# Performance work log

Hardware: AMD Instinct MI355X
Metric: run time of the kernel (lower is better)

Reference implementation:

```python
import jax, jax.numpy as jnp
import numpy as np

MAX_ITERS = 20
TOL = 1e-6
STEP = 1.0
EPS = 1e-7
CLIP = 1e-7


def _normalize(x, axis=-1):
    n = jnp.linalg.norm(x, axis=axis, keepdims=True)
    return x / jnp.maximum(n, 1e-12)


def _safe_acos(x):
    return jnp.arccos(jnp.clip(x, -1.0 + CLIP, 1.0 - CLIP))


def setup_inputs() -> dict:
    key = jax.random.key(0)
    NC, K, N, D = 1000, 8, 32, 128
    X_groups = jax.random.normal(key, (NC, K, N, D), dtype=jnp.float32)
    return {"X_groups": X_groups}


def reference(X_groups):
    # X_groups: (NC, K, N, D)
    NC, K, N, D = X_groups.shape
    X = X_groups.reshape(NC * K, N, D)
    Xn = _normalize(X)                      # (G, N, D) unit vectors
    mu = _normalize(jnp.mean(Xn, axis=1))   # (G, D) init mean

    done = jnp.array(False)
    for _ in range(MAX_ITERS):
        dots = jnp.einsum('gd,gnd->gn', mu, Xn)             # (G, N)
        theta = _safe_acos(dots)
        sin_t = jnp.maximum(jnp.sin(theta), EPS)
        diff = Xn - dots[..., None] * mu[:, None, :]        # (G, N, D)
        log_vecs = (theta / sin_t)[..., None] * diff        # log map
        v = jnp.mean(log_vecs, axis=1)                      # (G, D)
        v_norm = jnp.maximum(jnp.linalg.norm(v, axis=-1, keepdims=True), EPS)
        done = done | (jnp.max(v_norm) < TOL)               # global convergence (as in torch .item() check)
        v_step = STEP * v
        vs_norm = jnp.maximum(jnp.linalg.norm(v_step, axis=-1, keepdims=True), EPS)
        mu_new = jnp.cos(vs_norm) * mu + jnp.sin(vs_norm) * (v_step / vs_norm)  # exp map
        mu_new = _normalize(mu_new)
        mu = jnp.where(done, mu, mu_new)

    # calc_cluster_distance: features (G, N, D) @ means (G, D)
    sims = jnp.einsum('gnd,gd->gn', Xn, mu)
    sims = jnp.clip(sims, -1 + CLIP, 1 - CLIP)
    loss = jnp.mean(jnp.sum(jnp.arccos(sims) ** 2, axis=-1))
    return loss
```

## Files before the change

kernel.cpp:

```cpp
#include <hip/hip_runtime.h>
#include <stdint.h>

#define MAX_ITERS 20
#define EPSV 1e-7f
#define CLIPV 1e-7f
#define PI_F 3.14159265358979f
#define PIO2_F 1.57079632679490f

typedef __attribute__((ext_vector_type(8))) short short8;
typedef __attribute__((ext_vector_type(4))) float f4;

__device__ __forceinline__ f4 mfma_bf16(short8 a, short8 b, f4 c) {
    return __builtin_amdgcn_mfma_f32_16x16x32_bf16(a, b, c, 0, 0, 0);
}

template <int CTRL>
__device__ __forceinline__ float dpp_add(float v) {
    int p = __builtin_amdgcn_update_dpp(0, __float_as_int(v), CTRL, 0xF, 0xF, true);
    return v + __int_as_float(p);
}

__device__ __forceinline__ float halfsum32(float v) {
    v = dpp_add<0xB1>(v);
    v = dpp_add<0x4E>(v);
    v = dpp_add<0x141>(v);
    v = dpp_add<0x140>(v);
    int sw = __builtin_amdgcn_ds_swizzle(__float_as_int(v), 0x401F);
    return v + __int_as_float(sw);
}

__device__ __forceinline__ float bperm(int addr, int src) {
    return __int_as_float(__builtin_amdgcn_ds_bpermute(addr, src));
}

__device__ __forceinline__ float fast_acos(float x) {
    float a = fabsf(x);
    bool big = a > 0.5f;
    float z = big ? 0.5f * (1.0f - a) : x * x;
    float s = big ? sqrtf(z) : x;
    float p = fmaf(z, fmaf(z, fmaf(z, fmaf(z, 4.2163199048e-2f, 2.4181311049e-2f),
                                   4.5470025998e-2f), 7.4953002686e-2f),
                   1.6666752422e-1f);
    float r = fmaf(s * z, p, s);
    float big_val = (x < 0.0f) ? (PI_F - 2.0f * r) : (2.0f * r);
    return big ? big_val : (PIO2_F - r);
}

__device__ __forceinline__ void cvt_hilo(const float* v, short8& hi, short8& lo) {
#pragma unroll
    for (int i = 0; i < 8; ++i) {
        float x = v[i];
        uint32_t u = __float_as_uint(x);
        float hf = __uint_as_float(u & 0xFFFF0000u);
        float lf = x - hf;
        hi[i] = (short)(u >> 16);
        lo[i] = (short)(__float_as_uint(lf) >> 16);
    }
}

__global__ void __launch_bounds__(256, 4) karcher(const float* __restrict__ X,
                                                  float* __restrict__ ws,
                                                  int n_groups) {
    __shared__ float sG[8][32 * 33];
    __shared__ float sPart[8];

    const int lane = threadIdx.x & 63;
    const int wid  = threadIdx.x >> 6;
    const int g0   = blockIdx.x * 8 + wid * 2;
    if (threadIdx.x < 8) sPart[threadIdx.x] = 0.f;
    if (g0 >= n_groups) return;

    const int col  = lane & 15;
    const int quad = lane >> 4;

#pragma unroll
    for (int gg = 0; gg < 2; ++gg) {
        if (g0 + gg >= n_groups) break;
        const float* Xg = X + (size_t)(g0 + gg) * (32 * 128);
        f4 acc00 = {0.f, 0.f, 0.f, 0.f};
        f4 acc01 = acc00, acc10 = acc00, acc11 = acc00;
#pragma unroll
        for (int kc = 0; kc < 4; ++kc) {
            const float* p0 = Xg + col * 128 + kc * 32 + quad * 8;
            const float* p1 = p0 + 16 * 128;
            float r0[8], r1[8];
            *(float4*)(r0)     = *(const float4*)(p0);
            *(float4*)(r0 + 4) = *(const float4*)(p0 + 4);
            *(float4*)(r1)     = *(const float4*)(p1);
            *(float4*)(r1 + 4) = *(const float4*)(p1 + 4);
            short8 H0, L0, H1, L1;
            cvt_hilo(r0, H0, L0);
            cvt_hilo(r1, H1, L1);
            acc00 = mfma_bf16(H0, H0, acc00);
            acc00 = mfma_bf16(H0, L0, acc00);
            acc00 = mfma_bf16(L0, H0, acc00);
            acc01 = mfma_bf16(H0, H1, acc01);
            acc01 = mfma_bf16(H0, L1, acc01);
            acc01 = mfma_bf16(L0, H1, acc01);
            acc10 = mfma_bf16(H1, H0, acc10);
            acc10 = mfma_bf16(H1, L0, acc10);
            acc10 = mfma_bf16(L1, H0, acc10);
            acc11 = mfma_bf16(H1, H1, acc11);
            acc11 = mfma_bf16(H1, L1, acc11);
            acc11 = mfma_bf16(L1, H1, acc11);
        }
        float* Gw = sG[wid * 2 + gg];
#pragma unroll
        for (int i = 0; i < 4; ++i) {
            int rw = quad * 4 + i;
            Gw[rw * 33 + col]             = acc00[i];
            Gw[rw * 33 + col + 16]        = acc01[i];
            Gw[(rw + 16) * 33 + col]      = acc10[i];
            Gw[(rw + 16) * 33 + col + 16] = acc11[i];
        }
    }
    __syncthreads();

    const int half = lane >> 5;
    const int r    = lane & 31;
    const float* Gh = sG[wid * 2 + half];

    const int bbase = (lane & 32) << 2;
    int badr[32];
#pragma unroll
    for (int j = 0; j < 32; ++j) badr[j] = bbase | (j << 2);

    float d   = Gh[r * 34];
    float inv = 1.0f / fmaxf(sqrtf(d), 1e-12f);
    const int invb = __float_as_int(inv);

    float Grow[32];
#pragma unroll
    for (int j = 0; j < 32; ++j) {
        float invj = bperm(badr[j], invb);
        Grow[j] = Gh[r * 33 + j] * (inv * invj);
    }

    float a = 1.0f / 32.0f;
    float ga;
    {
        float s0 = 0, s1 = 0, s2 = 0, s3 = 0;
#pragma unroll
        for (int j = 0; j < 8; ++j) {
            s0 += Grow[j];
            s1 += Grow[j + 8];
            s2 += Grow[j + 16];
            s3 += Grow[j + 24];
        }
        ga = ((s0 + s1) + (s2 + s3)) * (1.0f / 32.0f);
        float n2   = halfsum32(a * ga);
        float inv0 = 1.0f / fmaxf(sqrtf(n2), 1e-12f);
        a  *= inv0;
        ga *= inv0;
    }

    for (int it = 0; it < MAX_ITERS; ++it) {
        float x  = fminf(fmaxf(ga, -1.0f + CLIPV), 1.0f - CLIPV);
        float th = fast_acos(x);
        float st = fmaxf(sqrtf(fmaxf(1.0f - x * x, 0.0f)), EPSV);
        float w  = __fdividef(th, st);
        float C  = halfsum32(w * ga);
        float beta = (w - C * a) * (1.0f / 32.0f);
        const int bi = __float_as_int(beta);
        float gb0 = 0, gb1 = 0, gb2 = 0, gb3 = 0;
#pragma unroll
        for (int j = 0; j < 8; ++j) {
            gb0 = fmaf(Grow[j],      bperm(badr[j],      bi), gb0);
            gb1 = fmaf(Grow[j + 8],  bperm(badr[j + 8],  bi), gb1);
            gb2 = fmaf(Grow[j + 16], bperm(badr[j + 16], bi), gb2);
            gb3 = fmaf(Grow[j + 24], bperm(badr[j + 24], bi), gb3);
        }
        float gb = (gb0 + gb1) + (gb2 + gb3);
        float vv = halfsum32(beta * gb);
        float vs = fmaxf(sqrtf(fmaxf(vv, 0.0f)), EPSV);
        float cv = __cosf(vs);
        float sv = __fdividef(__sinf(vs), vs);
        a  = fmaf(sv, beta, cv * a);
        ga = fmaf(sv, gb, cv * ga);
        if (__all(vs < 1e-6f)) break;
    }

    float xf = fminf(fmaxf(ga, -1.0f + CLIPV), 1.0f - CLIPV);
    float t  = fast_acos(xf);
    float ls = halfsum32(t * t);
    if (r == 0 && (g0 + half) < n_groups) sPart[wid * 2 + half] = ls;
    __syncthreads();
    if (threadIdx.x == 0) {
        float s = 0.f;
#pragma unroll
        for (int i = 0; i < 8; ++i) s += sPart[i];
        ws[blockIdx.x] = s;
    }
}

__global__ void __launch_bounds__(256) reduce_partials(const float* __restrict__ ws,
                                                       float* __restrict__ out,
                                                       int n, float scale) {
    __shared__ float sred[4];
    float s = 0.f;
    for (int i = threadIdx.x; i < n; i += 256) s += ws[i];
#pragma unroll
    for (int m = 32; m >= 1; m >>= 1) s += __shfl_xor(s, m, 64);
    const int lane = threadIdx.x & 63, wid = threadIdx.x >> 6;
    if (lane == 0) sred[wid] = s;
    __syncthreads();
    if (threadIdx.x == 0)
        out[0] = ((sred[0] + sred[1]) + (sred[2] + sred[3])) * scale;
}

extern "C" void kernel_launch(void* const* d_in, const int* in_sizes, int n_in,
                              void* d_out, int out_size, void* d_ws, size_t ws_size,
                              hipStream_t stream) {
    const float* X = (const float*)d_in[0];
    float* out = (float*)d_out;
    float* ws = (float*)d_ws;
    int n_groups = in_sizes[0] / (32 * 128);
    int blocks = (n_groups + 7) / 8;
    karcher<<<blocks, 256, 0, stream>>>(X, ws, n_groups);
    reduce_partials<<<1, 256, 0, stream>>>(ws, out, blocks, 1.0f / (float)n_groups);
}
```

Baseline: 217.9 us.

## Replace bpermute Gram-vector product with XOR-permuted DPP rotation scheme

Stores each lane's Gram row in XOR-permuted order so that the per-iteration matrix-vector product G·beta can walk the partner values with DPP quad/row moves instead of 32 ds_bpermute LDS operations. It computes G·w and derives G·beta algebraically from it (gb = (Gw - C·ga)/32), which removes the dependence on beta before the product. Half-wave reductions now use readlane instead of a swizzle. The inverse norms go through shared memory with an extra barrier. DPP row moves are cheap but serialised, and the changed summation order may slightly perturb numerics.

```diff
diff --git a/kernel.cpp b/kernel.cpp
--- a/kernel.cpp
+++ b/kernel.cpp
@@ -14,23 +14,39 @@
     return __builtin_amdgcn_mfma_f32_16x16x32_bf16(a, b, c, 0, 0, 0);
 }
 
+__device__ __forceinline__ float rl(float v, int l) {
+    return __int_as_float(__builtin_amdgcn_readlane(__float_as_int(v), l));
+}
+
 template <int CTRL>
 __device__ __forceinline__ float dpp_add(float v) {
     int p = __builtin_amdgcn_update_dpp(0, __float_as_int(v), CTRL, 0xF, 0xF, true);
     return v + __int_as_float(p);
 }
-
-__device__ __forceinline__ float halfsum32(float v) {
+template <int CTRL>
+__device__ __forceinline__ float dpp_mov(float v) {
+    return __int_as_float(__builtin_amdgcn_update_dpp(0, __float_as_int(v), CTRL, 0xF, 0xF, true));
+}
+
+__device__ __forceinline__ float rowsum16(float v) {
     v = dpp_add<0xB1>(v);
     v = dpp_add<0x4E>(v);
     v = dpp_add<0x141>(v);
     v = dpp_add<0x140>(v);
+    return v;
+}
+
+__device__ __forceinline__ float halfsum_rl(float v, bool hB) {
+    v = rowsum16(v);
+    float sA = rl(v, 0) + rl(v, 16);
+    float sB = rl(v, 32) + rl(v, 48);
+    return hB ? sB : sA;
+}
+
+__device__ __forceinline__ float halfsum_sw(float v) {
+    v = rowsum16(v);
     int sw = __builtin_amdgcn_ds_swizzle(__float_as_int(v), 0x401F);
     return v + __int_as_float(sw);
-}
-
-__device__ __forceinline__ float bperm(int addr, int src) {
-    return __int_as_float(__builtin_amdgcn_ds_bpermute(addr, src));
 }
 
 __device__ __forceinline__ float fast_acos(float x) {
@@ -58,10 +74,14 @@
     }
 }
 
+#define WSTEPA(CTRL, GI) { curA = dpp_mov<CTRL>(curA); accA = fmaf(Grow2[GI], curA, accA); }
+#define WSTEPB(CTRL, GI) { curB = dpp_mov<CTRL>(curB); accB = fmaf(Grow2[(GI) + 16], curB, accB); }
+
 __global__ void __launch_bounds__(256, 4) karcher(const float* __restrict__ X,
                                                   float* __restrict__ ws,
                                                   int n_groups) {
     __shared__ float sG[8][32 * 33];
+    __shared__ float sInv[8][32];
     __shared__ float sPart[8];
 
     const int lane = threadIdx.x & 63;
@@ -116,24 +136,21 @@
     }
     __syncthreads();
 
-    const int half = lane >> 5;
-    const int r    = lane & 31;
-    const float* Gh = sG[wid * 2 + half];
-
-    const int bbase = (lane & 32) << 2;
-    int badr[32];
-#pragma unroll
-    for (int j = 0; j < 32; ++j) badr[j] = bbase | (j << 2);
-
-    float d   = Gh[r * 34];
-    float inv = 1.0f / fmaxf(sqrtf(d), 1e-12f);
-    const int invb = __float_as_int(inv);
-
-    float Grow[32];
-#pragma unroll
-    for (int j = 0; j < 32; ++j) {
-        float invj = bperm(badr[j], invb);
-        Grow[j] = Gh[r * 33 + j] * (inv * invj);
+    const int  half = lane >> 5;
+    const bool hB   = half != 0;
+    const int  r    = lane & 31;
+    const float* Gh  = sG[wid * 2 + half];
+    float*       siH = sInv[wid * 2 + half];
+
+    float inv = 1.0f / fmaxf(sqrtf(Gh[r * 34]), 1e-12f);
+    siH[r] = inv;
+    __syncthreads();
+
+    float Grow2[32];
+#pragma unroll
+    for (int g = 0; g < 32; ++g) {
+        int j = r ^ g;
+        Grow2[g] = Gh[r * 33 + j] * (inv * siH[j]);
     }
 
     float a = 1.0f / 32.0f;
@@ -141,14 +158,14 @@
     {
         float s0 = 0, s1 = 0, s2 = 0, s3 = 0;
 #pragma unroll
-        for (int j = 0; j < 8; ++j) {
-            s0 += Grow[j];
-            s1 += Grow[j + 8];
-            s2 += Grow[j + 16];
-            s3 += Grow[j + 24];
+        for (int g = 0; g < 8; ++g) {
+            s0 += Grow2[g];
+            s1 += Grow2[g + 8];
+            s2 += Grow2[g + 16];
+            s3 += Grow2[g + 24];
         }
         ga = ((s0 + s1) + (s2 + s3)) * (1.0f / 32.0f);
-        float n2   = halfsum32(a * ga);
+        float n2   = halfsum_rl(a * ga, hB);
         float inv0 = 1.0f / fmaxf(sqrtf(n2), 1e-12f);
         a  *= inv0;
         ga *= inv0;
@@ -159,19 +176,30 @@
         float th = fast_acos(x);
         float st = fmaxf(sqrtf(fmaxf(1.0f - x * x, 0.0f)), EPSV);
         float w  = __fdividef(th, st);
-        float C  = halfsum32(w * ga);
-        float beta = (w - C * a) * (1.0f / 32.0f);
-        const int bi = __float_as_int(beta);
-        float gb0 = 0, gb1 = 0, gb2 = 0, gb3 = 0;
-#pragma unroll
-        for (int j = 0; j < 8; ++j) {
-            gb0 = fmaf(Grow[j],      bperm(badr[j],      bi), gb0);
-            gb1 = fmaf(Grow[j + 8],  bperm(badr[j + 8],  bi), gb1);
-            gb2 = fmaf(Grow[j + 16], bperm(badr[j + 16], bi), gb2);
-            gb3 = fmaf(Grow[j + 24], bperm(badr[j + 24], bi), gb3);
-        }
-        float gb = (gb0 + gb1) + (gb2 + gb3);
-        float vv = halfsum32(beta * gb);
+
+        int w16i = __builtin_amdgcn_ds_swizzle(__float_as_int(w), 0x401F);
+
+        float C = halfsum_sw(w * ga);
+
+        float curA = w;
+        float accA = Grow2[0] * curA;
+        WSTEPA(0xB1, 1)   WSTEPA(0x4E, 3)   WSTEPA(0xB1, 2)   WSTEPA(0x141, 6)
+        WSTEPA(0xB1, 7)   WSTEPA(0x4E, 5)   WSTEPA(0xB1, 4)   WSTEPA(0x140, 12)
+        WSTEPA(0xB1, 13)  WSTEPA(0x4E, 15)  WSTEPA(0xB1, 14)  WSTEPA(0x141, 10)
+        WSTEPA(0xB1, 11)  WSTEPA(0x4E, 9)   WSTEPA(0xB1, 8)
+
+        float curB = __int_as_float(w16i);
+        float accB = Grow2[16] * curB;
+        WSTEPB(0xB1, 1)   WSTEPB(0x4E, 3)   WSTEPB(0xB1, 2)   WSTEPB(0x141, 6)
+        WSTEPB(0xB1, 7)   WSTEPB(0x4E, 5)   WSTEPB(0xB1, 4)   WSTEPB(0x140, 12)
+        WSTEPB(0xB1, 13)  WSTEPB(0x4E, 15)  WSTEPB(0xB1, 14)  WSTEPB(0x141, 10)
+        WSTEPB(0xB1, 11)  WSTEPB(0x4E, 9)   WSTEPB(0xB1, 8)
+
+        float gw   = accA + accB;
+        float gb   = (gw - C * ga) * (1.0f / 32.0f);
+        float beta = (w  - C * a ) * (1.0f / 32.0f);
+
+        float vv = halfsum_rl(beta * gb, hB);
         float vs = fmaxf(sqrtf(fmaxf(vv, 0.0f)), EPSV);
         float cv = __cosf(vs);
         float sv = __fdividef(__sinf(vs), vs);
@@ -182,7 +210,7 @@
 
     float xf = fminf(fmaxf(ga, -1.0f + CLIPV), 1.0f - CLIPV);
     float t  = fast_acos(xf);
-    float ls = halfsum32(t * t);
+    float ls = halfsum_rl(t * t, hB);
     if (r == 0 && (g0 + half) < n_groups) sPart[wid * 2 + half] = ls;
     __syncthreads();
     if (threadIdx.x == 0) {
```

Measured after the change: 211.0 us. 3.1% less time.
